# Optimization experiments

Measured on AMD Instinct MI355X. Metric: run time of the kernel, lower is better.

The kernel has to match this reference:

```python
import jax, jax.numpy as jnp
import numpy as np

D = 1024      # d_model
H = 16        # nhead
DH = D // H   # head_dim = 64
ROT = DH // 2 # rotary_ndims = 32
FFN = 4096    # d_ffn
B, T, M, N = 4, 1024, 128, 64


def _layernorm(x, g, b, eps=1e-5):
    mu = jnp.mean(x, axis=-1, keepdims=True)
    var = jnp.mean(jnp.square(x - mu), axis=-1, keepdims=True)
    return (x - mu) * jax.lax.rsqrt(var + eps) * g + b


def _rotate_half(x):
    x1, x2 = x[..., : x.shape[-1] // 2], x[..., x.shape[-1] // 2:]
    return jnp.concatenate([-x2, x1], axis=-1)


def setup_inputs() -> dict:
    key = jax.random.key(0)
    ks = jax.random.split(key, 16)
    s = 0.02
    inp = {
        'x': jax.random.normal(ks[0], (B, T, D), jnp.float32),
        'memory': jax.random.normal(ks[1], (B, M, D), jnp.float32),
        'nmr': jax.random.normal(ks[2], (B, N, D), jnp.float32),
        'Wq': jax.random.normal(ks[3], (D, D), jnp.float32) * s,
        'bq': jnp.zeros((D,), jnp.float32),
        'Wk': jax.random.normal(ks[4], (D, D), jnp.float32) * s,
        'bk': jnp.zeros((D,), jnp.float32),
        'Wv': jax.random.normal(ks[5], (D, D), jnp.float32) * s,
        'bv': jnp.zeros((D,), jnp.float32),
        'Wo': jax.random.normal(ks[6], (D, D), jnp.float32) * s,
        'bo': jnp.zeros((D,), jnp.float32),
        'W1': jax.random.normal(ks[7], (D, FFN), jnp.float32) * s,
        'b1': jnp.zeros((FFN,), jnp.float32),
        'W2': jax.random.normal(ks[8], (FFN, D), jnp.float32) * s,
        'b2': jnp.zeros((D,), jnp.float32),
        'ln1_g': jnp.ones((D,), jnp.float32),
        'ln1_b': jnp.zeros((D,), jnp.float32),
        'ln2_g': jnp.ones((D,), jnp.float32),
        'ln2_b': jnp.zeros((D,), jnp.float32),
    }
    return inp


def reference(x, memory, nmr, Wq, bq, Wk, bk, Wv, bv, Wo, bo, W1, b1, W2, b2,
              ln1_g, ln1_b, ln2_g, ln2_b):
    b, t, _ = x.shape
    m, n = memory.shape[1], nmr.shape[1]
    pref = m + n
    L = pref + t

    x_full = jnp.concatenate([memory, nmr, x], axis=1)  # (B, L, D)
    xa = _layernorm(x_full, ln1_g, ln1_b)

    def heads(w, bias):
        return (xa @ w + bias).reshape(b, L, H, DH).transpose(0, 2, 1, 3)  # (B,H,L,DH)

    q = heads(Wq, bq)
    k = heads(Wk, bk)
    v = heads(Wv, bv)

    # partial RoPE on first ROT dims of each head
    pos = jnp.arange(L, dtype=jnp.float32)
    inv_freq = 1.0 / (10000.0 ** (jnp.arange(0, ROT, 2, dtype=jnp.float32) / ROT))
    freqs = pos[:, None] * inv_freq[None, :]              # (L, ROT/2)
    emb = jnp.concatenate([freqs, freqs], axis=-1)        # (L, ROT)
    cos, sin = jnp.cos(emb), jnp.sin(emb)
    qr, qp = q[..., :ROT], q[..., ROT:]
    kr, kp = k[..., :ROT], k[..., ROT:]
    qr = qr * cos + _rotate_half(qr) * sin
    kr = kr * cos + _rotate_half(kr) * sin
    q = jnp.concatenate([qr, qp], axis=-1)
    k = jnp.concatenate([kr, kp], axis=-1)

    # block mask: prefix (memory+nmr) fully bidirectional, target causal,
    # target attends to full prefix, prefix does NOT attend to target.
    i = jnp.arange(L)
    allowed = (i[None, :] < pref) | ((i[:, None] >= pref) & (i[None, :] >= pref)
                                     & (i[None, :] <= i[:, None]))  # (L, L)

    scale = 1.0 / jnp.sqrt(jnp.asarray(DH, jnp.float32))
    scores = jnp.einsum('bhqd,bhkd->bhqk', q, k) * scale
    scores = jnp.where(allowed[None, None], scores, jnp.finfo(scores.dtype).min)
    probs = jax.nn.softmax(scores, axis=-1)
    attn = jnp.einsum('bhqk,bhkd->bhqd', probs, v)        # (B,H,L,DH)
    attn = attn.transpose(0, 2, 1, 3).reshape(b, L, D)

    x_full = attn @ Wo + bo + x_full

    xf = _layernorm(x_full, ln2_g, ln2_b)
    xf = jnp.square(jax.nn.relu(xf @ W1 + b1)) @ W2 + b2
    x_full = x_full + xf

    return x_full[:, pref:]
```

## Files before the change

### kernel.cpp

```cpp
#include <hip/hip_runtime.h>
#include <hip/hip_bf16.h>
#include <math.h>

#define D_   1024
#define H_   16
#define DH_  64
#define FFN_ 4096
#define B_   4
#define T_   1024
#define M_   128
#define N_   64
#define PREF 192
#define L_   1216
#define BL_  (B_*L_)
#define BT_  (B_*T_)

typedef __attribute__((ext_vector_type(4))) float f32x4;
typedef __attribute__((ext_vector_type(8))) short bf16x8;
typedef __attribute__((ext_vector_type(8))) unsigned short u16x8;
typedef const __attribute__((address_space(1))) void gvoid_t;
typedef __attribute__((address_space(3))) void lvoid_t;

#define LGKM0 asm volatile("s_waitcnt lgkmcnt(0)" ::: "memory")
#define CFENCE asm volatile("" ::: "memory")

__device__ __forceinline__ void gl_lds16(const void* g, void* l) {
    __builtin_amdgcn_global_load_lds((gvoid_t*)g, (lvoid_t*)l, 16, 0, 0);
}

__device__ __forceinline__ ushort f2bf(float x) {
    union { __hip_bfloat16 h; ushort u; } cv;
    cv.h = __float2bfloat16(x);
    return cv.u;
}

__device__ __forceinline__ u16x8 pack8(float4 a, float4 b) {
    u16x8 r;
    r[0]=f2bf(a.x); r[1]=f2bf(a.y); r[2]=f2bf(a.z); r[3]=f2bf(a.w);
    r[4]=f2bf(b.x); r[5]=f2bf(b.y); r[6]=f2bf(b.z); r[7]=f2bf(b.w);
    return r;
}

__device__ __forceinline__ float block_reduce_sum256(float v, float* sbuf) {
#pragma unroll
    for (int o = 32; o > 0; o >>= 1) v += __shfl_xor(v, o, 64);
    int w = threadIdx.x >> 6;
    if ((threadIdx.x & 63) == 0) sbuf[w] = v;
    __syncthreads();
    float r = sbuf[0] + sbuf[1] + sbuf[2] + sbuf[3];
    __syncthreads();
    return r;
}

__device__ __forceinline__ void wtr_body(const float* __restrict__ W,
                                         ushort* __restrict__ Wt, int K, int Nc)
{
    __shared__ float tl[64][65];
    int c0 = blockIdx.x << 6, k0 = blockIdx.y << 6;
    int tid = threadIdx.x;
    int rr = tid >> 4, c4 = (tid & 15) << 2;
#pragma unroll
    for (int p = 0; p < 4; ++p) {
        int r = (p << 4) + rr;
        float4 v = *(const float4*)(W + (size_t)(k0 + r) * Nc + c0 + c4);
        tl[r][c4+0] = v.x; tl[r][c4+1] = v.y; tl[r][c4+2] = v.z; tl[r][c4+3] = v.w;
    }
    __syncthreads();
#pragma unroll
    for (int p = 0; p < 4; ++p) {
        int rT = (p << 4) + rr;
        ushort4 uv;
        uv.x = f2bf(tl[c4+0][rT]);
        uv.y = f2bf(tl[c4+1][rT]);
        uv.z = f2bf(tl[c4+2][rT]);
        uv.w = f2bf(tl[c4+3][rT]);
        *(ushort4*)(Wt + (size_t)(c0 + rT) * K + k0 + c4) = uv;
    }
}

__global__ __launch_bounds__(256) void wtr_kernel(
    const float* __restrict__ W, ushort* __restrict__ Wt, int K, int Nc)
{ wtr_body(W, Wt, K, Nc); }

__global__ __launch_bounds__(256) void wtr4_kernel(
    const float* __restrict__ W0, const float* __restrict__ W1,
    const float* __restrict__ W2, const float* __restrict__ W3,
    ushort* __restrict__ T0, ushort* __restrict__ T1,
    ushort* __restrict__ T2, ushort* __restrict__ T3)
{
    const float* W; ushort* T;
    switch (blockIdx.z) {
        case 0: W = W0; T = T0; break;
        case 1: W = W1; T = T1; break;
        case 2: W = W2; T = T2; break;
        default: W = W3; T = T3; break;
    }
    wtr_body(W, T, D_, D_);
}

__global__ __launch_bounds__(256) void prep_kernel(
    float* __restrict__ tab, const float* __restrict__ bq,
    const float* __restrict__ bk, const float* __restrict__ bv,
    float* __restrict__ ob)
{
    int i = blockIdx.x * 256 + threadIdx.x;
    if (i < L_ * 32) {
        int pos = i >> 5, idx = i & 31;
        int fi = idx & 15;
        float invf = exp2f(-(float)fi * 0.83048202372f);
        float th = (float)pos * invf;
        tab[i] = (idx < 16) ? cosf(th) : sinf(th);
    } else {
        int j = i - L_ * 32;
        if (j < 3072) {
            float v = (j < 1024) ? bq[j] : (j < 2048 ? bk[j - 1024] : bv[j - 2048]);
            ob[j] = v;
        }
    }
}

__global__ __launch_bounds__(256) void ln1_concat_kernel(
    const float* __restrict__ x, const float* __restrict__ mem,
    const float* __restrict__ nmr, const float* __restrict__ g,
    const float* __restrict__ be, float* __restrict__ x_full,
    ushort* __restrict__ xa_bf)
{
    __shared__ float sbuf[4];
    int row = blockIdx.x;
    int b = row / L_, pos = row % L_;
    const float* src;
    if (pos < M_)          src = mem + ((size_t)b*M_ + pos)      * D_;
    else if (pos < M_+N_)  src = nmr + ((size_t)b*N_ + (pos-M_)) * D_;
    else                   src = x   + ((size_t)b*T_ + (pos-PREF))*D_;

    int c = threadIdx.x << 2;
    float4 v = *(const float4*)(src + c);
    float s = v.x + v.y + v.z + v.w;
    s = block_reduce_sum256(s, sbuf);
    float mu = s * (1.0f / D_);
    float dx = v.x - mu, dy = v.y - mu, dz = v.z - mu, dw = v.w - mu;
    float q = dx*dx + dy*dy + dz*dz + dw*dw;
    q = block_reduce_sum256(q, sbuf);
    float inv = rsqrtf(q * (1.0f / D_) + 1e-5f);
    float4 gv = *(const float4*)(g + c);
    float4 bv = *(const float4*)(be + c);
    ushort4 o;
    o.x = f2bf(dx*inv*gv.x + bv.x);
    o.y = f2bf(dy*inv*gv.y + bv.y);
    o.z = f2bf(dz*inv*gv.z + bv.z);
    o.w = f2bf(dw*inv*gv.w + bv.w);
    *(float4*)(x_full + (size_t)row*D_ + c) = v;
    *(ushort4*)(xa_bf + (size_t)row*D_ + c) = o;
}

__global__ __launch_bounds__(256) void ln2_kernel(
    const float* __restrict__ src, const float* __restrict__ g,
    const float* __restrict__ be, ushort* __restrict__ dst)
{
    __shared__ float sbuf[4];
    int row = blockIdx.x;
    int c = threadIdx.x << 2;
    float4 v = *(const float4*)(src + (size_t)row*D_ + c);
    float s = v.x + v.y + v.z + v.w;
    s = block_reduce_sum256(s, sbuf);
    float mu = s * (1.0f / D_);
    float dx = v.x - mu, dy = v.y - mu, dz = v.z - mu, dw = v.w - mu;
    float q = dx*dx + dy*dy + dz*dz + dw*dw;
    q = block_reduce_sum256(q, sbuf);
    float inv = rsqrtf(q * (1.0f / D_) + 1e-5f);
    float4 gv = *(const float4*)(g + c);
    float4 bv = *(const float4*)(be + c);
    ushort4 o;
    o.x = f2bf(dx*inv*gv.x + bv.x);
    o.y = f2bf(dy*inv*gv.y + bv.y);
    o.z = f2bf(dz*inv*gv.z + bv.z);
    o.w = f2bf(dw*inv*gv.w + bv.w);
    *(ushort4*)(dst + (size_t)row*D_ + c) = o;
}

__global__ __launch_bounds__(256) void gemm_bf16_kernel(
    const ushort* __restrict__ A, const ushort* __restrict__ Bt,
    const float* __restrict__ bias, const float* __restrict__ rtab,
    void* __restrict__ Cout, int Nc, int Kstride, int Klen, int mode)
{
    __shared__ ushort SM[24576];
    char* SMb = (char*)SM;
    int tid = threadIdx.x;
    int lane = tid & 63, w = tid >> 6;
    int wm = w >> 1, wn = w & 1;
    int nx = gridDim.x;
    int flat = blockIdx.y * nx + blockIdx.x;
    int cpx = (nx * gridDim.y) >> 3;
    int sz = (flat & 7) * cpx + (flat >> 3);
    int row0 = (sz / nx) << 7, col0 = (sz % nx) << 7;
    int l15 = lane & 15, l4 = lane >> 4;

    f32x4 acc[4][4] = {};

    int r_a = tid >> 2;
    int sc  = tid & 3;
    int lcOff = (sc ^ ((r_a >> 1) & 3)) << 3;
    const ushort* Arow  = A  + (size_t)(row0 + r_a)      * Kstride;
    const ushort* Arow2 = A  + (size_t)(row0 + 64 + r_a) * Kstride;
    const ushort* Brow  = Bt + (size_t)(col0 + r_a)      * Kstride;
    const ushort* Brow2 = Bt + (size_t)(col0 + 64 + r_a) * Kstride;

#define STAGEQ(bb, k0rel)                                                    \
    do { char* Ab = SMb + (bb)*8192; char* Bb = SMb + 24576 + (bb)*8192;     \
        gl_lds16(Arow  + (k0rel) + lcOff, Ab + (tid << 4));                  \
        gl_lds16(Arow2 + (k0rel) + lcOff, Ab + 4096 + (tid << 4));           \
        gl_lds16(Brow  + (k0rel) + lcOff, Bb + (tid << 4));                  \
        gl_lds16(Brow2 + (k0rel) + lcOff, Bb + 4096 + (tid << 4));           \
    } while (0)

    int nIt = Klen >> 5;
    STAGEQ(0, 0);
    STAGEQ(1, 32);
    int cur = 0;
    for (int it = 0; it < nIt; ++it) {
        if (it + 2 < nIt) {
            int s2 = cur + 2; if (s2 >= 3) s2 -= 3;
            STAGEQ(s2, (it + 2) << 5);
            asm volatile("s_waitcnt vmcnt(8)" ::: "memory");
        } else if (it + 1 < nIt) {
            asm volatile("s_waitcnt vmcnt(4)" ::: "memory");
        } else {
            asm volatile("s_waitcnt vmcnt(0)" ::: "memory");
        }
        __builtin_amdgcn_s_barrier();
        CFENCE;
        const ushort* As = (const ushort*)(SMb + cur*8192);
        const ushort* Bs = (const ushort*)(SMb + 24576 + cur*8192);
        bf16x8 af[4], bfr[4];
#pragma unroll
        for (int i = 0; i < 4; ++i) {
            int ra = (wm << 6) + (i << 4) + l15;
            af[i]  = *(const bf16x8*)(&As[ra*32 + ((l4 ^ ((ra >> 1) & 3)) << 3)]);
            int rb = (wn << 6) + (i << 4) + l15;
            bfr[i] = *(const bf16x8*)(&Bs[rb*32 + ((l4 ^ ((rb >> 1) & 3)) << 3)]);
        }
#pragma unroll
        for (int i = 0; i < 4; ++i)
#pragma unroll
            for (int j = 0; j < 4; ++j)
                acc[i][j] = __builtin_amdgcn_mfma_f32_16x16x32_bf16(af[i], bfr[j], acc[i][j], 0, 0, 0);
        CFENCE;
        __builtin_amdgcn_s_barrier();
        cur = (cur + 1 == 3) ? 0 : cur + 1;
    }
#undef STAGEQ

    float bcol[4];
#pragma unroll
    for (int j = 0; j < 4; ++j) bcol[j] = bias[col0 + (wn << 6) + (j << 4) + l15];

    float* scr = (float*)SM + w * 1088;
    int rr = lane >> 2, cseg = lane & 3;
    int hh = ((col0 & 1023) + (wn << 6)) >> 6;
    int which = col0 >> 10;

#pragma unroll
    for (int i = 0; i < 4; ++i) {
        LGKM0;
#pragma unroll
        for (int j = 0; j < 4; ++j)
#pragma unroll
            for (int r = 0; r < 4; ++r)
                scr[((l4 << 2) + r)*68 + (j << 4) + l15] = acc[i][j][r] + bcol[j];
        LGKM0;
        int grow = row0 + (wm << 6) + (i << 4) + rr;

        if (which == 2) {
            int r0g = row0 + (wm << 6) + (i << 4);
            int bb = r0g / L_;
            int posb = r0g - bb * L_;
            float4 v0, v1, v2, v3;
            v0.x = scr[ 0*68 + lane]; v0.y = scr[ 1*68 + lane];
            v0.z = scr[ 2*68 + lane]; v0.w = scr[ 3*68 + lane];
            v1.x = scr[ 4*68 + lane]; v1.y = scr[ 5*68 + lane];
            v1.z = scr[ 6*68 + lane]; v1.w = scr[ 7*68 + lane];
            v2.x = scr[ 8*68 + lane]; v2.y = scr[ 9*68 + lane];
            v2.z = scr[10*68 + lane]; v2.w = scr[11*68 + lane];
            v3.x = scr[12*68 + lane]; v3.y = scr[13*68 + lane];
            v3.z = scr[14*68 + lane]; v3.w = scr[15*68 + lane];
            ushort* O = (ushort*)Cout + 2*(size_t)BL_*D_;
            size_t base = ((size_t)(bb*H_ + hh)*64 + lane)*L_ + posb;
            *(u16x8*)(O + base)     = pack8(v0, v1);
            *(u16x8*)(O + base + 8) = pack8(v2, v3);
        } else {
            int bb = grow / L_;
            int pos = grow - bb * L_;
            float4 a0 = *(float4*)&scr[rr*68 + (cseg << 4) + 0];
            float4 a1 = *(float4*)&scr[rr*68 + (cseg << 4) + 4];
            float4 a2 = *(float4*)&scr[rr*68 + (cseg << 4) + 8];
            float4 a3 = *(float4*)&scr[rr*68 + (cseg << 4) + 12];
            if (cseg < 2) {
                int oseg = cseg ^ 1;
                float4 p0 = *(float4*)&scr[rr*68 + (oseg << 4) + 0];
                float4 p1 = *(float4*)&scr[rr*68 + (oseg << 4) + 4];
                float4 p2 = *(float4*)&scr[rr*68 + (oseg << 4) + 8];
                float4 p3 = *(float4*)&scr[rr*68 + (oseg << 4) + 12];
                const float* tb = rtab + pos*32;
                float4 c0 = *(const float4*)(tb + 0),  c1 = *(const float4*)(tb + 4);
                float4 c2 = *(const float4*)(tb + 8),  c3 = *(const float4*)(tb + 12);
                float4 s0 = *(const float4*)(tb + 16), s1 = *(const float4*)(tb + 20);
                float4 s2 = *(const float4*)(tb + 24), s3 = *(const float4*)(tb + 28);
                float sg = (cseg == 0) ? -1.f : 1.f;
                a0.x = a0.x*c0.x + sg*p0.x*s0.x; a0.y = a0.y*c0.y + sg*p0.y*s0.y;
                a0.z = a0.z*c0.z + sg*p0.z*s0.z; a0.w = a0.w*c0.w + sg*p0.w*s0.w;
                a1.x = a1.x*c1.x + sg*p1.x*s1.x; a1.y = a1.y*c1.y + sg*p1.y*s1.y;
                a1.z = a1.z*c1.z + sg*p1.z*s1.z; a1.w = a1.w*c1.w + sg*p1.w*s1.w;
                a2.x = a2.x*c2.x + sg*p2.x*s2.x; a2.y = a2.y*c2.y + sg*p2.y*s2.y;
                a2.z = a2.z*c2.z + sg*p2.z*s2.z; a2.w = a2.w*c2.w + sg*p2.w*s2.w;
                a3.x = a3.x*c3.x + sg*p3.x*s3.x; a3.y = a3.y*c3.y + sg*p3.y*s3.y;
                a3.z = a3.z*c3.z + sg*p3.z*s3.z; a3.w = a3.w*c3.w + sg*p3.w*s3.w;
            }
            ushort* O = (ushort*)Cout + (size_t)which * ((size_t)BL_*D_);
            size_t base = (((size_t)(bb*H_ + hh)*L_ + pos) << 6) + (cseg << 4);
            *(u16x8*)(O + base)     = pack8(a0, a1);
            *(u16x8*)(O + base + 8) = pack8(a2, a3);
        }
    }
}

__global__ __launch_bounds__(512) void gemm_ffn1_kernel(
    const ushort* __restrict__ A, const ushort* __restrict__ Bt,
    const float* __restrict__ bias, void* __restrict__ Cout,
    int Nc, int Kstride, int Klen)
{
    __shared__ ushort SM[36864];
    char* SMb = (char*)SM;

    int tid = threadIdx.x;
    int lane = tid & 63, w = tid >> 6;
    int l15 = lane & 15, l4 = lane >> 4;

    int nx = gridDim.x;
    int flat = blockIdx.y * nx + blockIdx.x;
    int cpx = (nx * gridDim.y) >> 3;
    int sz = (flat & 7) * cpx + (flat >> 3);
    int row0 = (sz / nx) << 7, col0 = (sz % nx) << 8;

    int wm = w >> 2, wn = w & 3;

    f32x4 acc[4][4] = {};

    int rA = tid >> 2, scA = tid & 3;
    int lcA = (scA ^ ((rA >> 1) & 3)) << 3;
    const ushort* Ar = A + (size_t)(row0 + rA) * Kstride + lcA;
    int lcB1 = (scA ^ (((128 + rA) >> 1) & 3)) << 3;
    const ushort* Br0 = Bt + (size_t)(col0 + rA)       * Kstride + lcA;
    const ushort* Br1 = Bt + (size_t)(col0 + 128 + rA) * Kstride + lcB1;

#define STG1(bb, k0rel)                                                       \
    do {                                                                      \
        gl_lds16(Ar  + (k0rel), SMb + (bb)*8192 + (tid << 4));                \
        gl_lds16(Br0 + (k0rel), SMb + 24576 + (bb)*16384 + (tid << 4));       \
        gl_lds16(Br1 + (k0rel), SMb + 24576 + (bb)*16384 + 8192 + (tid << 4));\
    } while (0)

    int nIt = Klen >> 5;
    STG1(0, 0);
    STG1(1, 32);
    int cur = 0;
    for (int it = 0; it < nIt; ++it) {
        if (it + 2 < nIt) {
            int s2 = cur + 2; if (s2 >= 3) s2 -= 3;
            STG1(s2, (it + 2) << 5);
            asm volatile("s_waitcnt vmcnt(6)" ::: "memory");
        } else if (it + 1 < nIt) {
            asm volatile("s_waitcnt vmcnt(3)" ::: "memory");
        } else {
            asm volatile("s_waitcnt vmcnt(0)" ::: "memory");
        }
        __builtin_amdgcn_s_barrier();
        CFENCE;
        const ushort* As = (const ushort*)(SMb + cur*8192);
        const ushort* Bs = (const ushort*)(SMb + 24576 + cur*16384);
        bf16x8 af[4], bfr[4];
#pragma unroll
        for (int i = 0; i < 4; ++i) {
            int ra = (wm << 6) + (i << 4) + l15;
            af[i]  = *(const bf16x8*)(&As[ra*32 + ((l4 ^ ((ra >> 1) & 3)) << 3)]);
            int rb = (wn << 6) + (i << 4) + l15;
            bfr[i] = *(const bf16x8*)(&Bs[rb*32 + ((l4 ^ ((rb >> 1) & 3)) << 3)]);
        }
#pragma unroll
        for (int i = 0; i < 4; ++i)
#pragma unroll
            for (int j = 0; j < 4; ++j)
                acc[i][j] = __builtin_amdgcn_mfma_f32_16x16x32_bf16(af[i], bfr[j], acc[i][j], 0, 0, 0);
        CFENCE;
        __builtin_amdgcn_s_barrier();
        cur = (cur + 1 == 3) ? 0 : cur + 1;
    }
#undef STG1

    float bcol[4];
#pragma unroll
    for (int j = 0; j < 4; ++j) bcol[j] = bias[col0 + (wn << 6) + (j << 4) + l15];

    float* scr = (float*)SMb + w * 1088;
    int rr = lane >> 2, cseg = lane & 3;
    int colbase = col0 + (wn << 6);

#pragma unroll
    for (int i = 0; i < 4; ++i) {
        LGKM0;
#pragma unroll
        for (int j = 0; j < 4; ++j)
#pragma unroll
            for (int r = 0; r < 4; ++r) {
                float v = acc[i][j][r] + bcol[j];
                v = fmaxf(v, 0.f); v *= v;
                scr[((l4 << 2) + r)*68 + (j << 4) + l15] = v;
            }
        LGKM0;
        int grow = row0 + (wm << 6) + (i << 4) + rr;
        float4 q0 = *(float4*)&scr[rr*68 + (cseg << 4) + 0];
        float4 q1 = *(float4*)&scr[rr*68 + (cseg << 4) + 4];
        float4 q2 = *(float4*)&scr[rr*68 + (cseg << 4) + 8];
        float4 q3 = *(float4*)&scr[rr*68 + (cseg << 4) + 12];
        int gcol = colbase + (cseg << 4);
        ushort* O = (ushort*)Cout;
        *(u16x8*)(O + (size_t)grow*Nc + gcol)     = pack8(q0, q1);
        *(u16x8*)(O + (size_t)grow*Nc + gcol + 8) = pack8(q2, q3);
    }
}

__global__ __launch_bounds__(256) void gemm_sk2_kernel(
    const ushort* __restrict__ A, const ushort* __restrict__ Bt,
    const float* __restrict__ bias, const float* __restrict__ res,
    float* __restrict__ Cout, int Nc, int Kstride, int Klen, int mode)
{
    __shared__ ushort SM[36864];
    char* SMb = (char*)SM;
    int tid = threadIdx.x;
    int lane = tid & 63, w = tid >> 6;
    int l15 = lane & 15, l4 = lane >> 4;
    int g = w >> 1, wm = w & 1;

    int nx = gridDim.x;
    int flat = blockIdx.y * nx + blockIdx.x;
    int cpx = (nx * gridDim.y) >> 3;
    int sz = (flat & 7) * cpx + (flat >> 3);
    int row0 = (sz / nx) << 7, col0 = (sz % nx) << 6;

    f32x4 acc[4][4] = {};
    const int kl = Klen >> 1;
    const int kb = g * kl;

    int gt = tid & 127;
    int rB = gt >> 2, sc = gt & 3;
    const ushort* Abase = A  + (size_t)row0 * Kstride + kb;
    const ushort* Bbase = Bt + (size_t)col0 * Kstride + kb;
    char* ALg = SMb + g * 24576;
    char* BLg = SMb + 49152 + g * 12288;

#define STG2(bb, k0rel)                                                       \
    do {                                                                      \
        _Pragma("unroll")                                                     \
        for (int p = 0; p < 4; ++p) {                                         \
            int rw = (p << 5) + rB; int lc = sc ^ ((rw >> 1) & 3);            \
            gl_lds16(Abase + (size_t)rw*Kstride + (k0rel) + (lc << 3),        \
                     ALg + (bb)*8192 + (p << 11) + (gt << 4));                \
        }                                                                     \
        _Pragma("unroll")                                                     \
        for (int p = 0; p < 2; ++p) {                                         \
            int rw = (p << 5) + rB; int lc = sc ^ ((rw >> 1) & 3);            \
            gl_lds16(Bbase + (size_t)rw*Kstride + (k0rel) + (lc << 3),        \
                     BLg + (bb)*4096 + (p << 11) + (gt << 4));                \
        }                                                                     \
    } while (0)

    int nIt = kl >> 5;
    STG2(0, 0);
    STG2(1, 32);
    int cur = 0;
    for (int it = 0; it < nIt; ++it) {
        if (it + 2 < nIt) {
            int s2 = cur + 2; if (s2 >= 3) s2 -= 3;
            STG2(s2, (it + 2) << 5);
            asm volatile("s_waitcnt vmcnt(12)" ::: "memory");
        } else if (it + 1 < nIt) {
            asm volatile("s_waitcnt vmcnt(6)" ::: "memory");
        } else {
            asm volatile("s_waitcnt vmcnt(0)" ::: "memory");
        }
        __builtin_amdgcn_s_barrier();
        CFENCE;
        const ushort* As = (const ushort*)(ALg + cur*8192);
        const ushort* Bs = (const ushort*)(BLg + cur*4096);
        bf16x8 af[4], bfr[4];
#pragma unroll
        for (int i = 0; i < 4; ++i) {
            int ra = (wm << 6) + (i << 4) + l15;
            af[i]  = *(const bf16x8*)(&As[ra*32 + ((l4 ^ ((ra >> 1) & 3)) << 3)]);
            int rb = (i << 4) + l15;
            bfr[i] = *(const bf16x8*)(&Bs[rb*32 + ((l4 ^ ((rb >> 1) & 3)) << 3)]);
        }
#pragma unroll
        for (int i = 0; i < 4; ++i)
#pragma unroll
            for (int j = 0; j < 4; ++j)
                acc[i][j] = __builtin_amdgcn_mfma_f32_16x16x32_bf16(af[i], bfr[j], acc[i][j], 0, 0, 0);
        CFENCE;
        __builtin_amdgcn_s_barrier();
        cur = (cur + 1 == 3) ? 0 : cur + 1;
    }
#undef STG2

    float* scr2 = (float*)SMb;
    if (g == 1) {
#pragma unroll
        for (int i = 0; i < 4; ++i)
#pragma unroll
            for (int j = 0; j < 4; ++j)
#pragma unroll
                for (int r = 0; r < 4; ++r)
                    scr2[((wm << 6) + (i << 4) + (l4 << 2) + r)*68 + (j << 4) + l15] = acc[i][j][r];
    }
    __syncthreads();
    if (g == 1) return;
#pragma unroll
    for (int i = 0; i < 4; ++i)
#pragma unroll
        for (int j = 0; j < 4; ++j)
#pragma unroll
            for (int r = 0; r < 4; ++r)
                acc[i][j][r] += scr2[((wm << 6) + (i << 4) + (l4 << 2) + r)*68 + (j << 4) + l15];

    float bcol[4];
#pragma unroll
    for (int j = 0; j < 4; ++j) bcol[j] = bias[col0 + (j << 4) + l15];
    int rr = lane >> 2, cseg = lane & 3;
    float* scr = (float*)(SMb + 36864) + w * 1088;

#pragma unroll
    for (int i = 0; i < 4; ++i) {
        LGKM0;
#pragma unroll
        for (int j = 0; j < 4; ++j)
#pragma unroll
            for (int r = 0; r < 4; ++r)
                scr[((l4 << 2) + r)*68 + (j << 4) + l15] = acc[i][j][r] + bcol[j];
        LGKM0;
        int grow = row0 + (wm << 6) + (i << 4) + rr;
        float4 q0 = *(float4*)&scr[rr*68 + (cseg << 4) + 0];
        float4 q1 = *(float4*)&scr[rr*68 + (cseg << 4) + 4];
        float4 q2 = *(float4*)&scr[rr*68 + (cseg << 4) + 8];
        float4 q3 = *(float4*)&scr[rr*68 + (cseg << 4) + 12];
        int gcol = col0 + (cseg << 4);
        size_t roff;
        if (mode == 2) {
            int rs = (grow >> 10)*L_ + PREF + (grow & (T_-1));
            roff = (size_t)rs*D_ + gcol;
        } else {
            roff = (size_t)grow*Nc + gcol;
        }
        float4 r0 = *(const float4*)(res + roff);
        float4 r1 = *(const float4*)(res + roff + 4);
        float4 r2 = *(const float4*)(res + roff + 8);
        float4 r3 = *(const float4*)(res + roff + 12);
        q0.x += r0.x; q0.y += r0.y; q0.z += r0.z; q0.w += r0.w;
        q1.x += r1.x; q1.y += r1.y; q1.z += r1.z; q1.w += r1.w;
        q2.x += r2.x; q2.y += r2.y; q2.z += r2.z; q2.w += r2.w;
        q3.x += r3.x; q3.y += r3.y; q3.z += r3.z; q3.w += r3.w;
        size_t o = (size_t)grow*Nc + gcol;
        *(float4*)(Cout + o)      = q0;
        *(float4*)(Cout + o + 4)  = q1;
        *(float4*)(Cout + o + 8)  = q2;
        *(float4*)(Cout + o + 12) = q3;
    }
}

__global__ __launch_bounds__(256) void attn_mfma_kernel(
    const ushort* __restrict__ qhd, const ushort* __restrict__ khd,
    const ushort* __restrict__ vt, ushort* __restrict__ attn_bf)
{
    __shared__ ushort Ks[2][64*64];
    __shared__ ushort Vs[2][64*64];
    __shared__ ushort Ps[4*16*64];

    int bid0 = blockIdx.x;
    int bid = (bid0 & 7) * (gridDim.x >> 3) + (bid0 >> 3);
    int qb = 15 - (bid & 15);
    int h  = (bid >> 4) & (H_ - 1);
    int b  = bid >> 8;
    int tid = threadIdx.x, lane = tid & 63, w = tid >> 6;
    int l15 = lane & 15, lg = lane >> 4;
    int i0 = PREF + (qb << 6);
    int wq0 = w << 4;
    size_t bh = (size_t)(b * H_ + h);

    const ushort* qrow = qhd + (bh * L_ + i0 + wq0 + l15) * 64;
    bf16x8 bq0 = *(const bf16x8*)(qrow + (lg << 3));
    bf16x8 bq1 = *(const bf16x8*)(qrow + 32 + (lg << 3));

    f32x4 acc[4] = {};
    float mrun = -INFINITY;
    float lsum = 0.f;

    int srow = tid >> 3;
    int sslot = tid & 7;
    ushort* Ps_w = Ps + (w << 10);
    const float SC = 0.125f * 1.4426950408889634f;
    int qcap = i0 + wq0 + l15;

#define STAGE_T(buf, t)                                                     \
    do { int j0s = (t) << 6;                                                \
        gl_lds16(khd + (bh * L_ + j0s + srow) * 64 + ((sslot ^ (srow & 7)) << 3),      \
                 (char*)Ks[buf] + (tid << 4));                              \
        gl_lds16(khd + (bh * L_ + j0s + 32 + srow) * 64 + ((sslot ^ ((32+srow) & 7)) << 3), \
                 (char*)Ks[buf] + ((256 + tid) << 4));                      \
        gl_lds16(vt + (bh * 64 + srow) * L_ + j0s + ((sslot ^ (srow & 7)) << 3),       \
                 (char*)Vs[buf] + (tid << 4));                              \
        gl_lds16(vt + (bh * 64 + 32 + srow) * L_ + j0s + ((sslot ^ ((32+srow) & 7)) << 3), \
                 (char*)Vs[buf] + ((256 + tid) << 4));                      \
    } while (0)

    int ntile = 4 + qb;
    STAGE_T(0, 0);
    __syncthreads();
    int cur = 0;
    for (int t = 0; t < ntile; ++t) {
        if (t + 1 < ntile) STAGE_T(cur ^ 1, t + 1);
        const ushort* Kc = Ks[cur];
        const ushort* Vc = Vs[cur];

        f32x4 s4[4];
        __builtin_amdgcn_s_setprio(1);
#pragma unroll
        for (int st = 0; st < 4; ++st) {
            int rk = (st << 4) + l15;
            bf16x8 ak0 = *(const bf16x8*)(Kc + (rk << 6) + ((lg       ^ (rk & 7)) << 3));
            bf16x8 ak1 = *(const bf16x8*)(Kc + (rk << 6) + (((4 + lg) ^ (rk & 7)) << 3));
            f32x4 z = {};
            z = __builtin_amdgcn_mfma_f32_16x16x32_bf16(ak0, bq0, z, 0, 0, 0);
            z = __builtin_amdgcn_mfma_f32_16x16x32_bf16(ak1, bq1, z, 0, 0, 0);
            s4[st] = z;
        }
        __builtin_amdgcn_s_setprio(0);

        int j0 = t << 6;
        float sv[4][4];
        bool diag = (t == ntile - 1);
        int kbq = j0 + (lg << 2);
#pragma unroll
        for (int st = 0; st < 4; ++st)
#pragma unroll
            for (int r = 0; r < 4; ++r) {
                float s = s4[st][r] * SC;
                if (diag && (kbq + (st << 4) + r > qcap)) s = -INFINITY;
                sv[st][r] = s;
            }
        float bm;
        {
            float t0 = fmaxf(fmaxf(sv[0][0], sv[0][1]), fmaxf(sv[0][2], sv[0][3]));
            float t1 = fmaxf(fmaxf(sv[1][0], sv[1][1]), fmaxf(sv[1][2], sv[1][3]));
            float t2 = fmaxf(fmaxf(sv[2][0], sv[2][1]), fmaxf(sv[2][2], sv[2][3]));
            float t3 = fmaxf(fmaxf(sv[3][0], sv[3][1]), fmaxf(sv[3][2], sv[3][3]));
            bm = fmaxf(fmaxf(t0, t1), fmaxf(t2, t3));
        }
        bm = fmaxf(bm, __shfl_xor(bm, 16, 64));
        bm = fmaxf(bm, __shfl_xor(bm, 32, 64));

        float mn = fmaxf(mrun, bm);
        float cr = exp2f(mrun - mn);
        mrun = mn;
        float pe[4][4];
        float ps = 0.f;
#pragma unroll
        for (int st = 0; st < 4; ++st)
#pragma unroll
            for (int r = 0; r < 4; ++r) {
                float e = exp2f(sv[st][r] - mn);
                pe[st][r] = e; ps += e;
            }
        ps += __shfl_xor(ps, 16, 64);
        ps += __shfl_xor(ps, 32, 64);
        lsum = lsum * cr + ps;
#pragma unroll
        for (int su = 0; su < 4; ++su) acc[su] *= cr;

#pragma unroll
        for (int st = 0; st < 4; ++st) {
            int slot = (st << 1) + (lg >> 1);
            int sb = ((lg & 1) << 3);
#pragma unroll
            for (int rp = 0; rp < 2; ++rp) {
                uint u = (uint)f2bf(pe[st][2*rp]) | ((uint)f2bf(pe[st][2*rp+1]) << 16);
                *(uint*)((char*)Ps_w + l15*128 + ((slot ^ (l15 & 7)) << 4) + sb + (rp << 2)) = u;
            }
        }
        {
            bf16x8 bp0 = *(const bf16x8*)((char*)Ps_w + l15*128 + ((lg       ^ (l15 & 7)) << 4));
            bf16x8 bp1 = *(const bf16x8*)((char*)Ps_w + l15*128 + (((4 + lg) ^ (l15 & 7)) << 4));
            __builtin_amdgcn_s_setprio(1);
#pragma unroll
            for (int su = 0; su < 4; ++su) {
                int rd = (su << 4) + l15;
                bf16x8 av0 = *(const bf16x8*)(Vc + (rd << 6) + ((lg       ^ (rd & 7)) << 3));
                bf16x8 av1 = *(const bf16x8*)(Vc + (rd << 6) + (((4 + lg) ^ (rd & 7)) << 3));
                acc[su] = __builtin_amdgcn_mfma_f32_16x16x32_bf16(av0, bp0, acc[su], 0, 0, 0);
                acc[su] = __builtin_amdgcn_mfma_f32_16x16x32_bf16(av1, bp1, acc[su], 0, 0, 0);
            }
            __builtin_amdgcn_s_setprio(0);
        }
        __syncthreads();
        cur ^= 1;
    }
#undef STAGE_T

    float rl = 1.0f / lsum;
    size_t orow = (size_t)b * T_ + (i0 - PREF) + wq0 + l15;
#pragma unroll
    for (int su = 0; su < 4; ++su) {
        ushort4 o4;
        o4.x = f2bf(acc[su][0] * rl);
        o4.y = f2bf(acc[su][1] * rl);
        o4.z = f2bf(acc[su][2] * rl);
        o4.w = f2bf(acc[su][3] * rl);
        *(ushort4*)(attn_bf + orow * D_ + (h << 6) + (su << 4) + (lg << 2)) = o4;
    }
}

extern "C" void kernel_launch(void* const* d_in, const int* in_sizes, int n_in,
                              void* d_out, int out_size, void* d_ws, size_t ws_size,
                              hipStream_t stream) {
    const float* x   = (const float*)d_in[0];
    const float* mem = (const float*)d_in[1];
    const float* nmr = (const float*)d_in[2];
    const float* Wq  = (const float*)d_in[3];
    const float* bq  = (const float*)d_in[4];
    const float* Wk  = (const float*)d_in[5];
    const float* bk  = (const float*)d_in[6];
    const float* Wv  = (const float*)d_in[7];
    const float* bv  = (const float*)d_in[8];
    const float* Wo  = (const float*)d_in[9];
    const float* bo  = (const float*)d_in[10];
    const float* W1  = (const float*)d_in[11];
    const float* b1  = (const float*)d_in[12];
    const float* W2  = (const float*)d_in[13];
    const float* b2  = (const float*)d_in[14];
    const float* g1  = (const float*)d_in[15];
    const float* be1 = (const float*)d_in[16];
    const float* g2  = (const float*)d_in[17];
    const float* be2 = (const float*)d_in[18];
    float* out = (float*)d_out;

    const size_t BLD = (size_t)BL_ * D_;
    const size_t BTD = (size_t)BT_ * D_;

    float* f = (float*)d_ws;
    float* x_full = f;
    float* x2     = f + BLD;
    float* bqkv   = x2 + BTD;
    float* rtab   = bqkv + 4096;
    ushort* bfb   = (ushort*)(rtab + (size_t)L_*32);
    ushort* xa_bf   = bfb;
    ushort* qhd     = bfb + BLD;
    ushort* khd     = bfb + 2*BLD;
    ushort* vt      = bfb + 3*BLD;
    ushort* h1_bf   = bfb + 4*BLD;
    ushort* wq_bf = h1_bf + (size_t)BT_*FFN_;
    ushort* wk_bf = wq_bf + (size_t)D_*D_;
    ushort* wv_bf = wk_bf + (size_t)D_*D_;
    ushort* wo_bf = wv_bf + (size_t)D_*D_;
    ushort* w1_bf = wo_bf + (size_t)D_*D_;
    ushort* w2_bf = w1_bf + (size_t)D_*FFN_;
    ushort* attn_bf = xa_bf;
    ushort* ln2_bf  = qhd;

    wtr4_kernel<<<dim3(16, 16, 4), 256, 0, stream>>>(Wq, Wk, Wv, Wo,
                                                     wq_bf, wk_bf, wv_bf, wo_bf);
    wtr_kernel<<<dim3(FFN_/64, D_/64),   256, 0, stream>>>(W1, w1_bf, D_,   FFN_);
    wtr_kernel<<<dim3(D_/64,   FFN_/64), 256, 0, stream>>>(W2, w2_bf, FFN_, D_);
    prep_kernel<<<(L_*32 + 3072 + 255)/256, 256, 0, stream>>>(rtab, bq, bk, bv, bqkv);

    ln1_concat_kernel<<<BL_, 256, 0, stream>>>(x, mem, nmr, g1, be1, x_full, xa_bf);

    gemm_bf16_kernel<<<dim3(3072/128, BL_/128), 256, 0, stream>>>(
        xa_bf, wq_bf, bqkv, rtab, qhd, D_, D_, D_, 7);

    attn_mfma_kernel<<<B_*H_*(T_/64), 256, 0, stream>>>(qhd, khd, vt, attn_bf);

    gemm_sk2_kernel<<<dim3(D_/64, BT_/128), 256, 0, stream>>>(
        attn_bf, wo_bf, bo, x_full, x2, D_, D_, D_, 2);

    ln2_kernel<<<BT_, 256, 0, stream>>>(x2, g2, be2, ln2_bf);

    gemm_ffn1_kernel<<<dim3(FFN_/256, BT_/128), 512, 0, stream>>>(
        ln2_bf, w1_bf, b1, h1_bf, FFN_, D_, D_);

    gemm_sk2_kernel<<<dim3(D_/64, BT_/128), 256, 0, stream>>>(
        h1_bf, w2_bf, b2, x2, out, D_, FFN_, FFN_, 1);
}
```

Measured before the change: 250.4 us.

## Load K and V tiles directly from global memory in attention kernel

Drops the double-buffered LDS staging of K and V tiles and their block-level barriers in the attention kernel. Each wave now reads its MFMA operands for K and transposed V straight from global memory, relying on L1/L2 caching for reuse across the four waves. This cuts LDS usage, which may raise occupancy, and removes the per-tile __syncthreads. The cost is redundant global traffic across waves and the loss of load-compute overlap. The s_setprio hints are removed as well.

```diff
diff --git a/kernel.cpp b/kernel.cpp
--- a/kernel.cpp
+++ b/kernel.cpp
@@ -578,8 +578,6 @@
     const ushort* __restrict__ qhd, const ushort* __restrict__ khd,
     const ushort* __restrict__ vt, ushort* __restrict__ attn_bf)
 {
-    __shared__ ushort Ks[2][64*64];
-    __shared__ ushort Vs[2][64*64];
     __shared__ ushort Ps[4*16*64];
 
     int bid0 = blockIdx.x;
@@ -597,52 +595,31 @@
     bf16x8 bq0 = *(const bf16x8*)(qrow + (lg << 3));
     bf16x8 bq1 = *(const bf16x8*)(qrow + 32 + (lg << 3));
 
+    const ushort* Kb = khd + bh * (size_t)L_ * 64 + (lg << 3);
+    const ushort* Vb = vt + bh * (size_t)64 * L_;
+
     f32x4 acc[4] = {};
     float mrun = -INFINITY;
     float lsum = 0.f;
-
-    int srow = tid >> 3;
-    int sslot = tid & 7;
     ushort* Ps_w = Ps + (w << 10);
     const float SC = 0.125f * 1.4426950408889634f;
     int qcap = i0 + wq0 + l15;
 
-#define STAGE_T(buf, t)                                                     \
-    do { int j0s = (t) << 6;                                                \
-        gl_lds16(khd + (bh * L_ + j0s + srow) * 64 + ((sslot ^ (srow & 7)) << 3),      \
-                 (char*)Ks[buf] + (tid << 4));                              \
-        gl_lds16(khd + (bh * L_ + j0s + 32 + srow) * 64 + ((sslot ^ ((32+srow) & 7)) << 3), \
-                 (char*)Ks[buf] + ((256 + tid) << 4));                      \
-        gl_lds16(vt + (bh * 64 + srow) * L_ + j0s + ((sslot ^ (srow & 7)) << 3),       \
-                 (char*)Vs[buf] + (tid << 4));                              \
-        gl_lds16(vt + (bh * 64 + 32 + srow) * L_ + j0s + ((sslot ^ ((32+srow) & 7)) << 3), \
-                 (char*)Vs[buf] + ((256 + tid) << 4));                      \
-    } while (0)
-
     int ntile = 4 + qb;
-    STAGE_T(0, 0);
-    __syncthreads();
-    int cur = 0;
     for (int t = 0; t < ntile; ++t) {
-        if (t + 1 < ntile) STAGE_T(cur ^ 1, t + 1);
-        const ushort* Kc = Ks[cur];
-        const ushort* Vc = Vs[cur];
-
+        int j0 = t << 6;
         f32x4 s4[4];
-        __builtin_amdgcn_s_setprio(1);
 #pragma unroll
         for (int st = 0; st < 4; ++st) {
-            int rk = (st << 4) + l15;
-            bf16x8 ak0 = *(const bf16x8*)(Kc + (rk << 6) + ((lg       ^ (rk & 7)) << 3));
-            bf16x8 ak1 = *(const bf16x8*)(Kc + (rk << 6) + (((4 + lg) ^ (rk & 7)) << 3));
+            const ushort* kr = Kb + (size_t)(j0 + (st << 4) + l15) * 64;
+            bf16x8 ak0 = *(const bf16x8*)(kr);
+            bf16x8 ak1 = *(const bf16x8*)(kr + 32);
             f32x4 z = {};
             z = __builtin_amdgcn_mfma_f32_16x16x32_bf16(ak0, bq0, z, 0, 0, 0);
             z = __builtin_amdgcn_mfma_f32_16x16x32_bf16(ak1, bq1, z, 0, 0, 0);
             s4[st] = z;
         }
-        __builtin_amdgcn_s_setprio(0);
-
-        int j0 = t << 6;
+
         float sv[4][4];
         bool diag = (t == ntile - 1);
         int kbq = j0 + (lg << 2);
@@ -696,21 +673,16 @@
         {
             bf16x8 bp0 = *(const bf16x8*)((char*)Ps_w + l15*128 + ((lg       ^ (l15 & 7)) << 4));
             bf16x8 bp1 = *(const bf16x8*)((char*)Ps_w + l15*128 + (((4 + lg) ^ (l15 & 7)) << 4));
-            __builtin_amdgcn_s_setprio(1);
 #pragma unroll
             for (int su = 0; su < 4; ++su) {
-                int rd = (su << 4) + l15;
-                bf16x8 av0 = *(const bf16x8*)(Vc + (rd << 6) + ((lg       ^ (rd & 7)) << 3));
-                bf16x8 av1 = *(const bf16x8*)(Vc + (rd << 6) + (((4 + lg) ^ (rd & 7)) << 3));
+                const ushort* vr = Vb + (size_t)((su << 4) + l15) * L_ + j0 + (lg << 3);
+                bf16x8 av0 = *(const bf16x8*)(vr);
+                bf16x8 av1 = *(const bf16x8*)(vr + 32);
                 acc[su] = __builtin_amdgcn_mfma_f32_16x16x32_bf16(av0, bp0, acc[su], 0, 0, 0);
                 acc[su] = __builtin_amdgcn_mfma_f32_16x16x32_bf16(av1, bp1, acc[su], 0, 0, 0);
             }
-            __builtin_amdgcn_s_setprio(0);
-        }
-        __syncthreads();
-        cur ^= 1;
-    }
-#undef STAGE_T
+        }
+    }
 
     float rl = 1.0f / lsum;
     size_t orow = (size_t)b * T_ + (i0 - PREF) + wq0 + l15;
```

New measurement: 324.3 us. +29.5%, slower.
